# Performance work log

Hardware: AMD Instinct MI355X
Metric: run time of the kernel (lower is better)

The kernel has to match this reference:

```python
import jax, jax.numpy as jnp
import numpy as np

NUM_HEADS = 16


def _rope(x, c, s):
    # x: [T, H, D]; c, s: [T, D/2] -> rotate-half RoPE over full head_dim
    d2 = c.shape[-1]
    x1, x2 = x[..., :d2], x[..., d2:]
    c = c[:, None, :]
    s = s[:, None, :]
    return jnp.concatenate([x1 * c - x2 * s, x2 * c + x1 * s], axis=-1)


def setup_inputs() -> dict:
    key = jax.random.key(0)
    ks = jax.random.split(key, 4)
    B, L, dim = 8, 1024, 1024
    T = B * L
    D = dim // NUM_HEADS
    hidden_states = jax.random.normal(ks[0], (T, dim), dtype=jnp.float32)
    w_qkv = jax.random.normal(ks[1], (dim, 3 * dim), dtype=jnp.float32) * (dim ** -0.5)
    b_qkv = jnp.zeros((3 * dim,), dtype=jnp.float32)
    w_proj = jax.random.normal(ks[2], (dim, dim), dtype=jnp.float32) * (dim ** -0.5)
    b_proj = jnp.zeros((dim,), dtype=jnp.float32)
    # RoPE tables: positions restart at 0 for each packed sequence
    pos = jnp.tile(jnp.arange(L, dtype=jnp.float32), B)  # [T]
    inv_freq = 1.0 / (10000.0 ** (jnp.arange(0, D, 2, dtype=jnp.float32) / D))  # [D/2]
    freqs = pos[:, None] * inv_freq[None, :]  # [T, D/2]
    emb = jnp.concatenate([freqs, freqs], axis=-1)  # [T, D]
    cos = jnp.cos(emb)
    sin = jnp.sin(emb)
    cu_seqlens = (jnp.arange(B + 1, dtype=jnp.int32) * L)
    return {"hidden_states": hidden_states, "cos": cos, "sin": sin,
            "w_qkv": w_qkv, "b_qkv": b_qkv, "w_proj": w_proj, "b_proj": b_proj,
            "cu_seqlens": cu_seqlens}


def reference(hidden_states, cos, sin, w_qkv, b_qkv, w_proj, b_proj, cu_seqlens):
    T, dim = hidden_states.shape
    H = NUM_HEADS
    D = dim // H
    B = cu_seqlens.shape[0] - 1  # equal-length packed sequences
    L = T // B

    qkv = hidden_states @ w_qkv + b_qkv            # [T, 3*dim]
    qkv = qkv.reshape(T, 3, H, D)
    q, k, v = qkv[:, 0], qkv[:, 1], qkv[:, 2]       # [T, H, D]

    # module chunks cos/sin in half along last dim before apply_rotary_emb
    c = cos[..., : D // 2].astype(jnp.float32)
    s = sin[..., : D // 2].astype(jnp.float32)
    q = _rope(q.astype(jnp.float32), c, s).astype(hidden_states.dtype)
    k = _rope(k.astype(jnp.float32), c, s).astype(hidden_states.dtype)

    # varlen flash attention == block-diagonal attention; equal lengths -> reshape
    qb = q.reshape(B, L, H, D)
    kb = k.reshape(B, L, H, D)
    vb = v.reshape(B, L, H, D)
    scale = D ** -0.5
    scores = jnp.einsum("bqhd,bkhd->bhqk", qb, kb) * scale  # [B, H, L, L]
    probs = jax.nn.softmax(scores, axis=-1)
    out = jnp.einsum("bhqk,bkhd->bqhd", probs, vb)           # [B, L, H, D]
    out = out.reshape(T, dim)
    return out @ w_proj + b_proj
```

## Files before the change

### kernel.cpp

```cpp
#include <hip/hip_runtime.h>

typedef unsigned short ushort_t;
typedef __attribute__((ext_vector_type(8))) short short8;
typedef __attribute__((ext_vector_type(4))) float f32x4;

#define AS1 __attribute__((address_space(1)))
#define AS3 __attribute__((address_space(3)))

__device__ __forceinline__ ushort_t f2bf(float f) {
  unsigned int u = __builtin_bit_cast(unsigned int, f);
  u += 0x7fffu + ((u >> 16) & 1u);
  return (ushort_t)(u >> 16);
}

__device__ __forceinline__ unsigned int pack_bf2(float a, float b) {
  unsigned int ua = __builtin_bit_cast(unsigned int, a) + 0x8000u;
  unsigned int ub = __builtin_bit_cast(unsigned int, b) + 0x8000u;
  return (ua >> 16) | (ub & 0xffff0000u);
}

__device__ __forceinline__ void load_lds16(const ushort_t* g, ushort_t* l) {
  __builtin_amdgcn_global_load_lds((AS1 void*)g, (AS3 void*)l, 16, 0, 0);
}

#define MFMA16(a, b, c) __builtin_amdgcn_mfma_f32_16x16x32_bf16((a), (b), (c), 0, 0, 0)

__global__ __launch_bounds__(256) void k_convert(const float* __restrict__ src,
                                                 ushort_t* __restrict__ dst, int n8) {
  int i = blockIdx.x * 256 + threadIdx.x;
  if (i >= n8) return;
  const float4* s4 = (const float4*)src;
  float4 a = s4[(size_t)i * 2], b = s4[(size_t)i * 2 + 1];
  short8 o;
  o[0] = (short)f2bf(a.x); o[1] = (short)f2bf(a.y);
  o[2] = (short)f2bf(a.z); o[3] = (short)f2bf(a.w);
  o[4] = (short)f2bf(b.x); o[5] = (short)f2bf(b.y);
  o[6] = (short)f2bf(b.z); o[7] = (short)f2bf(b.w);
  *(short8*)(dst + (size_t)i * 8) = o;
}

__global__ __launch_bounds__(256) void k_transpose_w(const float* __restrict__ wqkv,
                                                     ushort_t* __restrict__ wqkvT,
                                                     const float* __restrict__ wproj,
                                                     ushort_t* __restrict__ wprojT) {
  __shared__ ushort_t t[64 * 65];
  const float* src;
  ushort_t* dst;
  int C, bx;
  if (blockIdx.x < 48) { src = wqkv; dst = wqkvT; C = 3072; bx = blockIdx.x; }
  else { src = wproj; dst = wprojT; C = 1024; bx = blockIdx.x - 48; }
  const int R = 1024;
  const int x0 = bx * 64, y0 = blockIdx.y * 64;
  const int c = threadIdx.x & 63, r0 = threadIdx.x >> 6;
#pragma unroll
  for (int i = 0; i < 16; ++i) {
    int r = r0 + i * 4;
    t[c * 65 + r] = f2bf(src[(size_t)(y0 + r) * C + x0 + c]);
  }
  __syncthreads();
#pragma unroll
  for (int i = 0; i < 16; ++i) {
    int rr = r0 + i * 4;
    dst[(size_t)(x0 + rr) * R + y0 + c] = t[rr * 65 + c];
  }
}

__global__ __launch_bounds__(512) void k_qkv_gemm_rope(
    const ushort_t* __restrict__ A, const ushort_t* __restrict__ Bt,
    const float* __restrict__ bias, const float* __restrict__ cosb,
    const float* __restrict__ sinb, ushort_t* __restrict__ Qb,
    ushort_t* __restrict__ Kb, ushort_t* __restrict__ Vb) {
  constexpr int K = 1024;
  __shared__ __align__(16) ushort_t As[256 * 64];
  __shared__ __align__(16) ushort_t Bs[128 * 64];
  const int tid = threadIdx.x, lane = tid & 63, wave = tid >> 6;
  const int quad = lane >> 4, ml = lane & 15;
  const int wm = wave & 3, wn = wave >> 2;
  const int m0 = blockIdx.y * 256, n0 = blockIdx.x * 128;
  f32x4 acc[4][4] = {};

  for (int kt = 0; kt < K / 64; ++kt) {
    __syncthreads();
    {
      const int kk0 = kt * 64;
#pragma unroll
      for (int i = 0; i < 4; ++i) {
        int cch = i * 512 + tid;
        int r = cch >> 3, s = cch & 7, gs = s ^ (r & 7);
        load_lds16(A + (size_t)(m0 + r) * K + kk0 + gs * 8, As + cch * 8);
      }
#pragma unroll
      for (int i = 0; i < 2; ++i) {
        int cch = i * 512 + tid;
        int r = cch >> 3, s = cch & 7, gs = s ^ (r & 7);
        load_lds16(Bt + (size_t)(n0 + r) * K + kk0 + gs * 8, Bs + cch * 8);
      }
    }
    __syncthreads();
#pragma unroll
    for (int ks = 0; ks < 2; ++ks) {
      short8 af[4], bfr[4];
#pragma unroll
      for (int mb = 0; mb < 4; ++mb) {
        int row = wm * 64 + mb * 16 + ml;
        int gs = (ks * 4 + quad) ^ (row & 7);
        af[mb] = *(const short8*)(As + row * 64 + gs * 8);
      }
#pragma unroll
      for (int nb = 0; nb < 4; ++nb) {
        int row = wn * 64 + nb * 16 + ml;
        int gs = (ks * 4 + quad) ^ (row & 7);
        bfr[nb] = *(const short8*)(Bs + row * 64 + gs * 8);
      }
#pragma unroll
      for (int mb = 0; mb < 4; ++mb)
#pragma unroll
        for (int nb = 0; nb < 4; ++nb)
          acc[mb][nb] = MFMA16(af[mb], bfr[nb], acc[mb][nb]);
    }
  }

  const int ncol0 = n0 + wn * 64;
  const int sec = ncol0 >> 10;
  const int h = (ncol0 & 1023) >> 6;
#pragma unroll
  for (int mb = 0; mb < 4; ++mb) {
#pragma unroll
    for (int rg = 0; rg < 4; ++rg) {
      const int m = m0 + wm * 64 + mb * 16 + quad * 4 + rg;
      const int b = m >> 10, l = m & 1023;
      const size_t ob = ((size_t)(b * 16 + h) * 1024 + l) * 64;
      if (sec < 2) {
        ushort_t* dst = (sec == 0) ? Qb : Kb;
#pragma unroll
        for (int nb = 0; nb < 2; ++nb) {
          const int d = nb * 16 + ml;
          float x1 = acc[mb][nb][rg] + bias[ncol0 + d];
          float x2 = acc[mb][nb + 2][rg] + bias[ncol0 + d + 32];
          float cv = cosb[(size_t)m * 64 + d];
          float sv = sinb[(size_t)m * 64 + d];
          dst[ob + d] = f2bf(x1 * cv - x2 * sv);
          dst[ob + d + 32] = f2bf(x2 * cv + x1 * sv);
        }
      } else {
#pragma unroll
        for (int nb = 0; nb < 4; ++nb) {
          const int d = nb * 16 + ml;
          Vb[ob + d] = f2bf(acc[mb][nb][rg] + bias[ncol0 + d]);
        }
      }
    }
  }
}

__global__ __launch_bounds__(256, 4) void k_attn(const ushort_t* __restrict__ Qb,
                                                 const ushort_t* __restrict__ Kb,
                                                 const ushort_t* __restrict__ Vb,
                                                 ushort_t* __restrict__ Ob) {
  __shared__ __align__(16) ushort_t QP[9216];
  __shared__ __align__(16) ushort_t Ks[64 * 64];
  __shared__ __align__(16) ushort_t Vts[64 * 72];
  const int tid = threadIdx.x, lane = tid & 63, wave = tid >> 6;
  const int quad = lane >> 4, ml = lane & 15;
  const int bh = blockIdx.x & 127, qt = blockIdx.x >> 7;
  const int q0 = qt * 128;
  const size_t base = (size_t)bh * (1024 * 64);
  const float CEXP = 0.18033688011112042f;

#pragma unroll
  for (int i = 0; i < 4; ++i) {
    int cch = i * 256 + tid;
    int r = cch >> 3, s = cch & 7, gs = s ^ (r & 7);
    load_lds16(Qb + base + (size_t)(q0 + r) * 64 + gs * 8, QP + cch * 8);
  }
  __syncthreads();

  short8 qf[2][2];
#pragma unroll
  for (int mb = 0; mb < 2; ++mb)
#pragma unroll
    for (int ks = 0; ks < 2; ++ks) {
      int row = wave * 32 + mb * 16 + ml;
      int gs = (ks * 4 + quad) ^ (row & 7);
      qf[mb][ks] = *(const short8*)(QP + row * 64 + gs * 8);
    }

  ushort_t* Pw = QP + wave * 2304;
  f32x4 Oacc[2][4] = {};
  float lsum[2][4] = {};

  for (int kt = 0; kt < 16; ++kt) {
    __syncthreads();
#pragma unroll
    for (int i = 0; i < 2; ++i) {
      int cch = i * 256 + tid;
      int r = cch >> 3, s = cch & 7, gs = s ^ (r & 7);
      load_lds16(Kb + base + (size_t)(kt * 64 + r) * 64 + gs * 8, Ks + cch * 8);
    }
    {
      const int k = tid & 63, d0 = (tid >> 6) * 16;
      const int c = (k & 15) * 4 + (k >> 4);
      const ushort_t* g = Vb + base + (size_t)(kt * 64 + k) * 64 + d0;
      short8 v0 = *(const short8*)g;
      short8 v1 = *(const short8*)(g + 8);
#pragma unroll
      for (int j = 0; j < 8; ++j) Vts[(d0 + j) * 72 + c] = (ushort_t)v0[j];
#pragma unroll
      for (int j = 0; j < 8; ++j) Vts[(d0 + 8 + j) * 72 + c] = (ushort_t)v1[j];
    }
    __syncthreads();

    f32x4 Sacc[2][4] = {};
#pragma unroll
    for (int nb = 0; nb < 4; ++nb)
#pragma unroll
      for (int ks = 0; ks < 2; ++ks) {
        int row = nb * 16 + ml;
        int gs = (ks * 4 + quad) ^ (row & 7);
        short8 kf = *(const short8*)(Ks + row * 64 + gs * 8);
        Sacc[0][nb] = MFMA16(qf[0][ks], kf, Sacc[0][nb]);
        Sacc[1][nb] = MFMA16(qf[1][ks], kf, Sacc[1][nb]);
      }

#pragma unroll
    for (int mb = 0; mb < 2; ++mb) {
#pragma unroll
      for (int rg = 0; rg < 4; ++rg) {
        float p0 = exp2f(Sacc[mb][0][rg] * CEXP);
        float p1 = exp2f(Sacc[mb][1][rg] * CEXP);
        float p2 = exp2f(Sacc[mb][2][rg] * CEXP);
        float p3 = exp2f(Sacc[mb][3][rg] * CEXP);
        lsum[mb][rg] += (p0 + p1) + (p2 + p3);
        uint2 w;
        w.x = pack_bf2(p0, p1);
        w.y = pack_bf2(p2, p3);
        *(uint2*)(Pw + (mb * 16 + quad * 4 + rg) * 72 + ml * 4) = w;
      }
    }

#pragma unroll
    for (int ks = 0; ks < 2; ++ks) {
      short8 pf[2];
#pragma unroll
      for (int mb = 0; mb < 2; ++mb)
        pf[mb] = *(const short8*)(Pw + (mb * 16 + ml) * 72 + ks * 32 + quad * 8);
#pragma unroll
      for (int nb = 0; nb < 4; ++nb) {
        short8 vf = *(const short8*)(Vts + (nb * 16 + ml) * 72 + ks * 32 + quad * 8);
        Oacc[0][nb] = MFMA16(pf[0], vf, Oacc[0][nb]);
        Oacc[1][nb] = MFMA16(pf[1], vf, Oacc[1][nb]);
      }
    }
  }

  const int b = bh >> 4, h = bh & 15;
#pragma unroll
  for (int mb = 0; mb < 2; ++mb) {
#pragma unroll
    for (int rg = 0; rg < 4; ++rg) {
      float l = lsum[mb][rg];
      l += __shfl_xor(l, 1);
      l += __shfl_xor(l, 2);
      l += __shfl_xor(l, 4);
      l += __shfl_xor(l, 8);
      float inv = 1.f / l;
      int q = q0 + wave * 32 + mb * 16 + quad * 4 + rg;
      size_t ob = ((size_t)(b * 1024 + q)) * 1024 + h * 64;
#pragma unroll
      for (int nb = 0; nb < 4; ++nb)
        Ob[ob + nb * 16 + ml] = f2bf(Oacc[mb][nb][rg] * inv);
    }
  }
}

__global__ __launch_bounds__(256) void k_proj_gemm(const ushort_t* __restrict__ A,
                                                   const ushort_t* __restrict__ Bt,
                                                   const float* __restrict__ bias,
                                                   float* __restrict__ out) {
  constexpr int K = 1024;
  __shared__ __align__(16) ushort_t As[128 * 64];
  __shared__ __align__(16) ushort_t Bs[128 * 64];
  const int tid = threadIdx.x, lane = tid & 63, wave = tid >> 6;
  const int quad = lane >> 4, ml = lane & 15;
  const int wm = wave & 1, wn = wave >> 1;
  const int m0 = blockIdx.y * 128, n0 = blockIdx.x * 128;
  f32x4 acc[4][4] = {};

  for (int kt = 0; kt < K / 64; ++kt) {
    __syncthreads();
    {
      const int kk0 = kt * 64;
#pragma unroll
      for (int i = 0; i < 4; ++i) {
        int cch = i * 256 + tid;
        int r = cch >> 3, s = cch & 7, gs = s ^ (r & 7);
        load_lds16(A + (size_t)(m0 + r) * K + kk0 + gs * 8, As + cch * 8);
        load_lds16(Bt + (size_t)(n0 + r) * K + kk0 + gs * 8, Bs + cch * 8);
      }
    }
    __syncthreads();
#pragma unroll
    for (int ks = 0; ks < 2; ++ks) {
      short8 af[4], bfr[4];
#pragma unroll
      for (int mb = 0; mb < 4; ++mb) {
        int row = wm * 64 + mb * 16 + ml;
        int gs = (ks * 4 + quad) ^ (row & 7);
        af[mb] = *(const short8*)(As + row * 64 + gs * 8);
      }
#pragma unroll
      for (int nb = 0; nb < 4; ++nb) {
        int row = wn * 64 + nb * 16 + ml;
        int gs = (ks * 4 + quad) ^ (row & 7);
        bfr[nb] = *(const short8*)(Bs + row * 64 + gs * 8);
      }
#pragma unroll
      for (int mb = 0; mb < 4; ++mb)
#pragma unroll
        for (int nb = 0; nb < 4; ++nb)
          acc[mb][nb] = MFMA16(af[mb], bfr[nb], acc[mb][nb]);
    }
  }
#pragma unroll
  for (int mb = 0; mb < 4; ++mb) {
#pragma unroll
    for (int rg = 0; rg < 4; ++rg) {
      const int m = m0 + wm * 64 + mb * 16 + quad * 4 + rg;
#pragma unroll
      for (int nb = 0; nb < 4; ++nb) {
        const int n = n0 + wn * 64 + nb * 16 + ml;
        out[(size_t)m * 1024 + n] = acc[mb][nb][rg] + bias[n];
      }
    }
  }
}

extern "C" void kernel_launch(void* const* d_in, const int* in_sizes, int n_in,
                              void* d_out, int out_size, void* d_ws, size_t ws_size,
                              hipStream_t stream) {
  const float* hs = (const float*)d_in[0];
  const float* cosb = (const float*)d_in[1];
  const float* sinb = (const float*)d_in[2];
  const float* wqkv = (const float*)d_in[3];
  const float* bqkv = (const float*)d_in[4];
  const float* wproj = (const float*)d_in[5];
  const float* bproj = (const float*)d_in[6];
  float* out = (float*)d_out;

  char* ws = (char*)d_ws;
  ushort_t* hsb = (ushort_t*)(ws);
  ushort_t* wqkvT = (ushort_t*)(ws + (16u << 20));
  ushort_t* wprojT = (ushort_t*)(ws + (22u << 20));
  ushort_t* Qb = (ushort_t*)(ws + (24u << 20));
  ushort_t* Kb = (ushort_t*)(ws + (40u << 20));
  ushort_t* Vb = (ushort_t*)(ws + (56u << 20));
  ushort_t* attnb = hsb;

  k_convert<<<4096, 256, 0, stream>>>(hs, hsb, 1048576);
  k_transpose_w<<<dim3(64, 16), 256, 0, stream>>>(wqkv, wqkvT, wproj, wprojT);
  k_qkv_gemm_rope<<<dim3(24, 32), 512, 0, stream>>>(hsb, wqkvT, bqkv, cosb, sinb,
                                                    Qb, Kb, Vb);
  k_attn<<<1024, 256, 0, stream>>>(Qb, Kb, Vb, attnb);
  k_proj_gemm<<<dim3(8, 64), 256, 0, stream>>>(attnb, wprojT, bproj, out);
}
```

Measured before the change: 265.6 us.

## Store V pre-transposed from QKV GEMM and enlarge attention query tile

The QKV GEMM epilogue now writes V in a transposed, key-permuted layout, so the attention kernel can load V tiles into LDS with async global-to-LDS copies instead of a register scatter transpose. The attention kernel also doubles its query tile to 256 rows per block (64 per wave), halving the grid and reusing each K/V tile across twice as many queries. The cost is more accumulator registers and LDS per block, with occupancy lowered to 2 blocks per CU in the launch bounds.

After: 292.4 us. 10.1% more time.

```diff
diff --git a/kernel.cpp b/kernel.cpp
--- a/kernel.cpp
+++ b/kernel.cpp
@@ -69,7 +69,7 @@
     const ushort_t* __restrict__ A, const ushort_t* __restrict__ Bt,
     const float* __restrict__ bias, const float* __restrict__ cosb,
     const float* __restrict__ sinb, ushort_t* __restrict__ Qb,
-    ushort_t* __restrict__ Kb, ushort_t* __restrict__ Vb) {
+    ushort_t* __restrict__ Kb, ushort_t* __restrict__ Vp) {
   constexpr int K = 1024;
   __shared__ __align__(16) ushort_t As[256 * 64];
   __shared__ __align__(16) ushort_t Bs[128 * 64];
@@ -123,15 +123,15 @@
   const int ncol0 = n0 + wn * 64;
   const int sec = ncol0 >> 10;
   const int h = (ncol0 & 1023) >> 6;
-#pragma unroll
-  for (int mb = 0; mb < 4; ++mb) {
-#pragma unroll
-    for (int rg = 0; rg < 4; ++rg) {
-      const int m = m0 + wm * 64 + mb * 16 + quad * 4 + rg;
-      const int b = m >> 10, l = m & 1023;
-      const size_t ob = ((size_t)(b * 16 + h) * 1024 + l) * 64;
-      if (sec < 2) {
-        ushort_t* dst = (sec == 0) ? Qb : Kb;
+  if (sec < 2) {
+    ushort_t* dst = (sec == 0) ? Qb : Kb;
+#pragma unroll
+    for (int mb = 0; mb < 4; ++mb) {
+#pragma unroll
+      for (int rg = 0; rg < 4; ++rg) {
+        const int m = m0 + wm * 64 + mb * 16 + quad * 4 + rg;
+        const int b = m >> 10, l = m & 1023;
+        const size_t ob = ((size_t)(b * 16 + h) * 1024 + l) * 64;
 #pragma unroll
         for (int nb = 0; nb < 2; ++nb) {
           const int d = nb * 16 + ml;
@@ -142,52 +142,63 @@
           dst[ob + d] = f2bf(x1 * cv - x2 * sv);
           dst[ob + d + 32] = f2bf(x2 * cv + x1 * sv);
         }
-      } else {
-#pragma unroll
-        for (int nb = 0; nb < 4; ++nb) {
-          const int d = nb * 16 + ml;
-          Vb[ob + d] = f2bf(acc[mb][nb][rg] + bias[ncol0 + d]);
-        }
-      }
-    }
-  }
-}
-
-__global__ __launch_bounds__(256, 4) void k_attn(const ushort_t* __restrict__ Qb,
+      }
+    }
+  } else {
+    const int mrow = m0 + wm * 64;
+    const int b = mrow >> 10, lB = mrow & 1023;
+    ushort_t* vb = Vp + ((size_t)(b * 16 + h)) * 65536 + lB;
+#pragma unroll
+    for (int rg = 0; rg < 4; ++rg) {
+#pragma unroll
+      for (int nb = 0; nb < 4; ++nb) {
+        const int d = nb * 16 + ml;
+        const float bs = bias[ncol0 + d];
+        uint2 w;
+        w.x = pack_bf2(acc[0][nb][rg] + bs, acc[1][nb][rg] + bs);
+        w.y = pack_bf2(acc[2][nb][rg] + bs, acc[3][nb][rg] + bs);
+        *(uint2*)(vb + (size_t)d * 1024 + 16 * quad + 4 * rg) = w;
+      }
+    }
+  }
+}
+
+__global__ __launch_bounds__(256, 2) void k_attn(const ushort_t* __restrict__ Qb,
                                                  const ushort_t* __restrict__ Kb,
-                                                 const ushort_t* __restrict__ Vb,
+                                                 const ushort_t* __restrict__ Vp,
                                                  ushort_t* __restrict__ Ob) {
-  __shared__ __align__(16) ushort_t QP[9216];
-  __shared__ __align__(16) ushort_t Ks[64 * 64];
-  __shared__ __align__(16) ushort_t Vts[64 * 72];
+  __shared__ __align__(16) ushort_t SM[26624];
+  ushort_t* Qs = SM;
+  ushort_t* Ks = SM + 18432;
+  ushort_t* Vts = SM + 22528;
   const int tid = threadIdx.x, lane = tid & 63, wave = tid >> 6;
   const int quad = lane >> 4, ml = lane & 15;
   const int bh = blockIdx.x & 127, qt = blockIdx.x >> 7;
-  const int q0 = qt * 128;
-  const size_t base = (size_t)bh * (1024 * 64);
+  const int q0 = qt * 256;
+  const size_t base = (size_t)bh * 65536;
   const float CEXP = 0.18033688011112042f;
 
 #pragma unroll
-  for (int i = 0; i < 4; ++i) {
+  for (int i = 0; i < 8; ++i) {
     int cch = i * 256 + tid;
     int r = cch >> 3, s = cch & 7, gs = s ^ (r & 7);
-    load_lds16(Qb + base + (size_t)(q0 + r) * 64 + gs * 8, QP + cch * 8);
+    load_lds16(Qb + base + (size_t)(q0 + r) * 64 + gs * 8, Qs + cch * 8);
   }
   __syncthreads();
 
-  short8 qf[2][2];
-#pragma unroll
-  for (int mb = 0; mb < 2; ++mb)
+  short8 qf[4][2];
+#pragma unroll
+  for (int mb = 0; mb < 4; ++mb)
 #pragma unroll
     for (int ks = 0; ks < 2; ++ks) {
-      int row = wave * 32 + mb * 16 + ml;
+      int row = wave * 64 + mb * 16 + ml;
       int gs = (ks * 4 + quad) ^ (row & 7);
-      qf[mb][ks] = *(const short8*)(QP + row * 64 + gs * 8);
-    }
-
-  ushort_t* Pw = QP + wave * 2304;
-  f32x4 Oacc[2][4] = {};
-  float lsum[2][4] = {};
+      qf[mb][ks] = *(const short8*)(Qs + row * 64 + gs * 8);
+    }
+
+  ushort_t* Pw = SM + wave * 4608;
+  f32x4 Oacc[4][4] = {};
+  float lsum[4][4] = {};
 
   for (int kt = 0; kt < 16; ++kt) {
     __syncthreads();
@@ -197,20 +208,15 @@
       int r = cch >> 3, s = cch & 7, gs = s ^ (r & 7);
       load_lds16(Kb + base + (size_t)(kt * 64 + r) * 64 + gs * 8, Ks + cch * 8);
     }
-    {
-      const int k = tid & 63, d0 = (tid >> 6) * 16;
-      const int c = (k & 15) * 4 + (k >> 4);
-      const ushort_t* g = Vb + base + (size_t)(kt * 64 + k) * 64 + d0;
-      short8 v0 = *(const short8*)g;
-      short8 v1 = *(const short8*)(g + 8);
-#pragma unroll
-      for (int j = 0; j < 8; ++j) Vts[(d0 + j) * 72 + c] = (ushort_t)v0[j];
-#pragma unroll
-      for (int j = 0; j < 8; ++j) Vts[(d0 + 8 + j) * 72 + c] = (ushort_t)v1[j];
-    }
-    __syncthreads();
-
-    f32x4 Sacc[2][4] = {};
+#pragma unroll
+    for (int i = 0; i < 2; ++i) {
+      int cch = i * 256 + tid;
+      int r = cch >> 3, s = cch & 7, gs = s ^ (r & 7);
+      load_lds16(Vp + base + (size_t)r * 1024 + kt * 64 + gs * 8, Vts + cch * 8);
+    }
+    __syncthreads();
+
+    f32x4 Sacc[4][4] = {};
 #pragma unroll
     for (int nb = 0; nb < 4; ++nb)
 #pragma unroll
@@ -218,12 +224,13 @@
         int row = nb * 16 + ml;
         int gs = (ks * 4 + quad) ^ (row & 7);
         short8 kf = *(const short8*)(Ks + row * 64 + gs * 8);
-        Sacc[0][nb] = MFMA16(qf[0][ks], kf, Sacc[0][nb]);
-        Sacc[1][nb] = MFMA16(qf[1][ks], kf, Sacc[1][nb]);
-      }
-
-#pragma unroll
-    for (int mb = 0; mb < 2; ++mb) {
+#pragma unroll
+        for (int mb = 0; mb < 4; ++mb)
+          Sacc[mb][nb] = MFMA16(qf[mb][ks], kf, Sacc[mb][nb]);
+      }
+
+#pragma unroll
+    for (int mb = 0; mb < 4; ++mb) {
 #pragma unroll
       for (int rg = 0; rg < 4; ++rg) {
         float p0 = exp2f(Sacc[mb][0][rg] * CEXP);
@@ -240,22 +247,25 @@
 
 #pragma unroll
     for (int ks = 0; ks < 2; ++ks) {
-      short8 pf[2];
-#pragma unroll
-      for (int mb = 0; mb < 2; ++mb)
+      short8 pf[4];
+#pragma unroll
+      for (int mb = 0; mb < 4; ++mb)
         pf[mb] = *(const short8*)(Pw + (mb * 16 + ml) * 72 + ks * 32 + quad * 8);
 #pragma unroll
       for (int nb = 0; nb < 4; ++nb) {
-        short8 vf = *(const short8*)(Vts + (nb * 16 + ml) * 72 + ks * 32 + quad * 8);
-        Oacc[0][nb] = MFMA16(pf[0], vf, Oacc[0][nb]);
-        Oacc[1][nb] = MFMA16(pf[1], vf, Oacc[1][nb]);
+        int row = nb * 16 + ml;
+        int gs = (ks * 4 + quad) ^ (row & 7);
+        short8 vf = *(const short8*)(Vts + row * 64 + gs * 8);
+#pragma unroll
+        for (int mb = 0; mb < 4; ++mb)
+          Oacc[mb][nb] = MFMA16(pf[mb], vf, Oacc[mb][nb]);
       }
     }
   }
 
   const int b = bh >> 4, h = bh & 15;
 #pragma unroll
-  for (int mb = 0; mb < 2; ++mb) {
+  for (int mb = 0; mb < 4; ++mb) {
 #pragma unroll
     for (int rg = 0; rg < 4; ++rg) {
       float l = lsum[mb][rg];
@@ -264,7 +274,7 @@
       l += __shfl_xor(l, 4);
       l += __shfl_xor(l, 8);
       float inv = 1.f / l;
-      int q = q0 + wave * 32 + mb * 16 + quad * 4 + rg;
+      int q = q0 + wave * 64 + mb * 16 + quad * 4 + rg;
       size_t ob = ((size_t)(b * 1024 + q)) * 1024 + h * 64;
 #pragma unroll
       for (int nb = 0; nb < 4; ++nb)
@@ -353,13 +363,13 @@
   ushort_t* wprojT = (ushort_t*)(ws + (22u << 20));
   ushort_t* Qb = (ushort_t*)(ws + (24u << 20));
   ushort_t* Kb = (ushort_t*)(ws + (40u << 20));
-  ushort_t* Vb = (ushort_t*)(ws + (56u << 20));
+  ushort_t* Vp = (ushort_t*)(ws + (56u << 20));
   ushort_t* attnb = hsb;
 
   k_convert<<<4096, 256, 0, stream>>>(hs, hsb, 1048576);
   k_transpose_w<<<dim3(64, 16), 256, 0, stream>>>(wqkv, wqkvT, wproj, wprojT);
   k_qkv_gemm_rope<<<dim3(24, 32), 512, 0, stream>>>(hsb, wqkvT, bqkv, cosb, sinb,
-                                                    Qb, Kb, Vb);
-  k_attn<<<1024, 256, 0, stream>>>(Qb, Kb, Vb, attnb);
+                                                    Qb, Kb, Vp);
+  k_attn<<<512, 256, 0, stream>>>(Qb, Kb, Vp, attnb);
   k_proj_gemm<<<dim3(8, 64), 256, 0, stream>>>(attnb, wprojT, bproj, out);
 }
```

## Store V transposed and permuted from QKV GEMM epilogue, async-load into attention LDS

Applied to the files above, without the earlier changes.

The QKV GEMM epilogue now writes V in a transposed per-head layout [d][l], packing four rows per 8-byte store in the order the PV MFMA expects. The attention kernel then loads V tiles directly into swizzled LDS with global_load_lds, instead of doing scalar LDS transposes every tile. This removes per-tile transpose work and LDS bank conflicts from the attention inner loop. In exchange the V writes in the GEMM epilogue are strided by 1024 elements, which may coalesce less well.

Result: faster. 257.3 us (-3.1%).

```diff
diff --git a/kernel.cpp b/kernel.cpp
--- a/kernel.cpp
+++ b/kernel.cpp
@@ -69,7 +69,7 @@
     const ushort_t* __restrict__ A, const ushort_t* __restrict__ Bt,
     const float* __restrict__ bias, const float* __restrict__ cosb,
     const float* __restrict__ sinb, ushort_t* __restrict__ Qb,
-    ushort_t* __restrict__ Kb, ushort_t* __restrict__ Vb) {
+    ushort_t* __restrict__ Kb, ushort_t* __restrict__ Vp) {
   constexpr int K = 1024;
   __shared__ __align__(16) ushort_t As[256 * 64];
   __shared__ __align__(16) ushort_t Bs[128 * 64];
@@ -123,15 +123,15 @@
   const int ncol0 = n0 + wn * 64;
   const int sec = ncol0 >> 10;
   const int h = (ncol0 & 1023) >> 6;
-#pragma unroll
-  for (int mb = 0; mb < 4; ++mb) {
-#pragma unroll
-    for (int rg = 0; rg < 4; ++rg) {
-      const int m = m0 + wm * 64 + mb * 16 + quad * 4 + rg;
-      const int b = m >> 10, l = m & 1023;
-      const size_t ob = ((size_t)(b * 16 + h) * 1024 + l) * 64;
-      if (sec < 2) {
-        ushort_t* dst = (sec == 0) ? Qb : Kb;
+  if (sec < 2) {
+    ushort_t* dst = (sec == 0) ? Qb : Kb;
+#pragma unroll
+    for (int mb = 0; mb < 4; ++mb) {
+#pragma unroll
+      for (int rg = 0; rg < 4; ++rg) {
+        const int m = m0 + wm * 64 + mb * 16 + quad * 4 + rg;
+        const int b = m >> 10, l = m & 1023;
+        const size_t ob = ((size_t)(b * 16 + h) * 1024 + l) * 64;
 #pragma unroll
         for (int nb = 0; nb < 2; ++nb) {
           const int d = nb * 16 + ml;
@@ -142,12 +142,22 @@
           dst[ob + d] = f2bf(x1 * cv - x2 * sv);
           dst[ob + d + 32] = f2bf(x2 * cv + x1 * sv);
         }
-      } else {
-#pragma unroll
-        for (int nb = 0; nb < 4; ++nb) {
-          const int d = nb * 16 + ml;
-          Vb[ob + d] = f2bf(acc[mb][nb][rg] + bias[ncol0 + d]);
-        }
+      }
+    }
+  } else {
+    const int mrow = m0 + wm * 64;
+    const int b = mrow >> 10, lB = mrow & 1023;
+    ushort_t* vb = Vp + ((size_t)(b * 16 + h)) * 65536 + lB;
+#pragma unroll
+    for (int rg = 0; rg < 4; ++rg) {
+#pragma unroll
+      for (int nb = 0; nb < 4; ++nb) {
+        const int d = nb * 16 + ml;
+        const float bs = bias[ncol0 + d];
+        uint2 w;
+        w.x = pack_bf2(acc[0][nb][rg] + bs, acc[1][nb][rg] + bs);
+        w.y = pack_bf2(acc[2][nb][rg] + bs, acc[3][nb][rg] + bs);
+        *(uint2*)(vb + (size_t)d * 1024 + 16 * quad + 4 * rg) = w;
       }
     }
   }
@@ -155,16 +165,16 @@
 
 __global__ __launch_bounds__(256, 4) void k_attn(const ushort_t* __restrict__ Qb,
                                                  const ushort_t* __restrict__ Kb,
-                                                 const ushort_t* __restrict__ Vb,
+                                                 const ushort_t* __restrict__ Vp,
                                                  ushort_t* __restrict__ Ob) {
   __shared__ __align__(16) ushort_t QP[9216];
   __shared__ __align__(16) ushort_t Ks[64 * 64];
-  __shared__ __align__(16) ushort_t Vts[64 * 72];
+  __shared__ __align__(16) ushort_t Vts[64 * 64];
   const int tid = threadIdx.x, lane = tid & 63, wave = tid >> 6;
   const int quad = lane >> 4, ml = lane & 15;
   const int bh = blockIdx.x & 127, qt = blockIdx.x >> 7;
   const int q0 = qt * 128;
-  const size_t base = (size_t)bh * (1024 * 64);
+  const size_t base = (size_t)bh * 65536;
   const float CEXP = 0.18033688011112042f;
 
 #pragma unroll
@@ -197,16 +207,11 @@
       int r = cch >> 3, s = cch & 7, gs = s ^ (r & 7);
       load_lds16(Kb + base + (size_t)(kt * 64 + r) * 64 + gs * 8, Ks + cch * 8);
     }
-    {
-      const int k = tid & 63, d0 = (tid >> 6) * 16;
-      const int c = (k & 15) * 4 + (k >> 4);
-      const ushort_t* g = Vb + base + (size_t)(kt * 64 + k) * 64 + d0;
-      short8 v0 = *(const short8*)g;
-      short8 v1 = *(const short8*)(g + 8);
-#pragma unroll
-      for (int j = 0; j < 8; ++j) Vts[(d0 + j) * 72 + c] = (ushort_t)v0[j];
-#pragma unroll
-      for (int j = 0; j < 8; ++j) Vts[(d0 + 8 + j) * 72 + c] = (ushort_t)v1[j];
+#pragma unroll
+    for (int i = 0; i < 2; ++i) {
+      int cch = i * 256 + tid;
+      int r = cch >> 3, s = cch & 7, gs = s ^ (r & 7);
+      load_lds16(Vp + base + (size_t)r * 1024 + kt * 64 + gs * 8, Vts + cch * 8);
     }
     __syncthreads();
 
@@ -246,7 +251,9 @@
         pf[mb] = *(const short8*)(Pw + (mb * 16 + ml) * 72 + ks * 32 + quad * 8);
 #pragma unroll
       for (int nb = 0; nb < 4; ++nb) {
-        short8 vf = *(const short8*)(Vts + (nb * 16 + ml) * 72 + ks * 32 + quad * 8);
+        int row = nb * 16 + ml;
+        int gs = (ks * 4 + quad) ^ (row & 7);
+        short8 vf = *(const short8*)(Vts + row * 64 + gs * 8);
         Oacc[0][nb] = MFMA16(pf[0], vf, Oacc[0][nb]);
         Oacc[1][nb] = MFMA16(pf[1], vf, Oacc[1][nb]);
       }
@@ -353,13 +360,13 @@
   ushort_t* wprojT = (ushort_t*)(ws + (22u << 20));
   ushort_t* Qb = (ushort_t*)(ws + (24u << 20));
   ushort_t* Kb = (ushort_t*)(ws + (40u << 20));
-  ushort_t* Vb = (ushort_t*)(ws + (56u << 20));
+  ushort_t* Vp = (ushort_t*)(ws + (56u << 20));
   ushort_t* attnb = hsb;
 
   k_convert<<<4096, 256, 0, stream>>>(hs, hsb, 1048576);
   k_transpose_w<<<dim3(64, 16), 256, 0, stream>>>(wqkv, wqkvT, wproj, wprojT);
   k_qkv_gemm_rope<<<dim3(24, 32), 512, 0, stream>>>(hsb, wqkvT, bqkv, cosb, sinb,
-                                                    Qb, Kb, Vb);
-  k_attn<<<1024, 256, 0, stream>>>(Qb, Kb, Vb, attnb);
+                                                    Qb, Kb, Vp);
+  k_attn<<<1024, 256, 0, stream>>>(Qb, Kb, Vp, attnb);
   k_proj_gemm<<<dim3(8, 64), 256, 0, stream>>>(attnb, wprojT, bproj, out);
 }
```
